# Performance work log

Hardware: AMD Instinct MI355X
Metric: run time of the kernel (lower is better)

## Reference

```python
import jax, jax.numpy as jnp
import numpy as np

K = 16                       # target expected number of distinct classes
NUM_LEVELS = 128             # num_discretization_levels
EPSILON = 0.1                # smoothing for derivative scales
NEWTON_ITERS = 3


def compute_normalizer(probs, k):
    """Solve for alpha s.t. sum_i (1 - exp(-alpha * p_i)) == k via Newton."""
    n = probs.shape[-1]
    alpha = jnp.full(probs.shape[:-1], float(k), dtype=probs.dtype)
    for _ in range(NEWTON_ITERS):
        e = jnp.exp(-alpha[..., None] * probs)          # (*, N)
        err = e.sum(axis=-1) + (k - n)                   # (*,)
        minus_d = (e * probs).sum(axis=-1)               # (*,)
        alpha = alpha + err / minus_d
    return alpha


def _derivative_scales(probs, eps):
    inv_p1 = 0.5 / (probs + eps)
    inv_p2 = 0.5 / (1.0 + eps - probs)
    common = eps * (inv_p1 + inv_p2)
    return inv_p1 + common, inv_p2 + common


@jax.custom_vjp
def fake_parameterized_dropout(probs, values, mask):
    return values * mask


def _fpd_fwd(probs, values, mask):
    return values * mask, (probs, values, mask)


def _fpd_bwd(res, g):
    probs, values, mask = res
    mask_grad = g * values
    s1, s2 = _derivative_scales(probs, EPSILON)
    probs_grad = mask_grad * (s1 * mask + s2 * (1.0 - mask))
    values_grad = g * mask
    return probs_grad, values_grad, jnp.zeros_like(mask)


fake_parameterized_dropout.defvjp(_fpd_fwd, _fpd_bwd)


def setup_inputs() -> dict:
    key = jax.random.key(0)
    k1, k2, k3, k4 = jax.random.split(key, 4)
    B, S, N = 4, 4096, 512
    return {
        "logits": jax.random.normal(k1, (B, S, N), dtype=jnp.float32),
        "values": jax.random.normal(k2, (B, S, N), dtype=jnp.float32),
        "u_mask": jax.random.uniform(k3, (B, S, N), dtype=jnp.float32),
        "u_disc": jax.random.uniform(k4, (B, S, N), dtype=jnp.float32),
    }


def reference(logits, values, u_mask, u_disc):
    probs = jax.nn.softmax(logits, axis=-1)                      # (*, N)
    alpha = compute_normalizer(probs, K)                         # (*,)
    # marginal prob of each class being chosen in K rounds
    marginals = 1.0 - (1.0 - probs) ** alpha[..., None]          # (*, N)
    # stochastic discretization with straight-through gradient
    idx = jnp.floor(marginals * (NUM_LEVELS - 1) + u_disc)
    y = idx * (1.0 / (NUM_LEVELS - 1))
    y_st = marginals + jax.lax.stop_gradient(y - marginals)
    # sample 0/1 mask with marginal probabilities y_st
    mask = (u_mask < y_st).astype(values.dtype)
    out = fake_parameterized_dropout(y_st, values, mask)
    return out
```

## Files before the change

kernel.cpp:

```cpp
#include <hip/hip_runtime.h>
#include <math.h>


#define ROW_N 512
#define EPW 16
constexpr double LEVELS_M1 = 127.0;
constexpr double INV_LEVELS_M1 = 1.0 / 127.0;

typedef float v4f __attribute__((ext_vector_type(4)));

template <int CTRL>
__device__ __forceinline__ float dpp_f32(float v) {
    int x = __builtin_amdgcn_update_dpp(0, __float_as_int(v), CTRL, 0xF, 0xF, true);
    return __int_as_float(x);
}
template <int CTRL>
__device__ __forceinline__ double dpp_f64(double v) {
    long long b = __double_as_longlong(v);
    int lo = __builtin_amdgcn_update_dpp(0, (int)(b & 0xFFFFFFFFLL), CTRL, 0xF, 0xF, true);
    int hi = __builtin_amdgcn_update_dpp(0, (int)(b >> 32),          CTRL, 0xF, 0xF, true);
    return __longlong_as_double(((long long)hi << 32) | (unsigned int)(unsigned)lo);
}

__device__ __forceinline__ double half_sum_f64(double v) {
    v += dpp_f64<0xB1>(v);
    v += dpp_f64<0x4E>(v);
    v += dpp_f64<0x141>(v);
    v += dpp_f64<0x140>(v);
    v += __shfl_xor(v, 16, 64);
    return v;
}
__device__ __forceinline__ float half_sum_f32(float v) {
    v += dpp_f32<0xB1>(v);
    v += dpp_f32<0x4E>(v);
    v += dpp_f32<0x141>(v);
    v += dpp_f32<0x140>(v);
    v += __shfl_xor(v, 16, 64);
    return v;
}

__device__ __forceinline__ double fast_recip1(double d) {
    double y = (double)__builtin_amdgcn_rcpf((float)d);
    return y * fma(-d, y, 2.0);
}

template <int DEG>
__device__ __forceinline__ double fast_exp(double x) {
    constexpr double C[12] = {
        1.0, 1.0, 0.5,
        1.6666666666666666574e-01,
        4.1666666666666664354e-02,
        8.3333333333333332177e-03,
        1.3888888888888889419e-03,
        1.9841269841269841253e-04,
        2.4801587301587301566e-05,
        2.7557319223985892511e-06,
        2.7557319223985888276e-07,
        2.5052108385441718775e-08
    };
    const double LOG2E = 1.4426950408889634074;
    const double LN2   = 6.9314718055994530942e-01;
    double kd = rint(x * LOG2E);
    double r  = fma(-kd, LN2, x);
    double p = C[DEG];
    #pragma unroll
    for (int k = DEG - 1; k >= 0; --k) p = fma(p, r, C[k]);
    long long sb = ((long long)(1023 + (int)kd)) << 52;
    return p * __longlong_as_double(sb);
}

__device__ __forceinline__ double fast_log1p(double r) {
    double u  = r * fast_recip1(2.0 + r);
    double u2 = u * u;
    double q = 2.0 / 9.0;
    q = fma(q, u2, 2.0 / 7.0);
    q = fma(q, u2, 2.0 / 5.0);
    q = fma(q, u2, 2.0 / 3.0);
    q = fma(q, u2, 2.0);
    return u * q;
}

__global__ __launch_bounds__(256)
void sbm_kernel(const float* __restrict__ logits,
                const float* __restrict__ values,
                const float* __restrict__ u_mask,
                const float* __restrict__ u_disc,
                float* __restrict__ out,
                int rows)
{
    const int wave = (int)((blockIdx.x * (unsigned)blockDim.x + threadIdx.x) >> 6);
    const int lane = (int)(threadIdx.x & 63u);
    if (2 * wave >= rows) return;

    const int half = lane >> 5;
    const int c    = lane & 31;

    const size_t pb = (size_t)wave * 256;
    const int    fi = half * 128 + c;

    const float4* l4 = (const float4*)logits + pb + fi;
    const float4* v4 = (const float4*)values + pb + fi;
    const float4* m4 = (const float4*)u_mask + pb + fi;
    const float4* d4 = (const float4*)u_disc + pb + fi;

    float4 lg[4], vv[4], um[4], ud[4];
    #pragma unroll
    for (int g = 0; g < 4; ++g) {
        lg[g] = l4[g * 32];
        vv[g] = v4[g * 32];
        um[g] = m4[g * 32];
        ud[g] = d4[g * 32];
    }

    double p[EPW];
    double s = 0.0;
    #pragma unroll
    for (int g = 0; g < 4; ++g) {
        const float lf[4] = {lg[g].x, lg[g].y, lg[g].z, lg[g].w};
        #pragma unroll
        for (int j = 0; j < 4; ++j) {
            p[g * 4 + j] = fast_exp<7>((double)lf[j]);
            s += p[g * 4 + j];
        }
    }
    s = half_sum_f64(s);
    const double inv_s = fast_recip1(s);
    float p32[EPW];
    #pragma unroll
    for (int i = 0; i < EPW; ++i) {
        p[i] *= inv_s;
        p32[i] = (float)p[i];
    }

    float se32 = 0.0f, sep32 = 0.0f;
    #pragma unroll
    for (int i = 0; i < EPW; ++i) {
        float e = __expf(-16.0f * p32[i]);
        se32 += e;
        sep32 = fmaf(e, p32[i], sep32);
    }
    se32  = half_sum_f32(se32);
    sep32 = half_sum_f32(sep32);
    const float a32 = 16.0f + (se32 - 496.0f) / sep32;

    double alpha = (double)a32;
    {
        double se = 0.0;
        float  sepf = 0.0f;
        #pragma unroll
        for (int i = 0; i < EPW; ++i) {
            double e = fast_exp<9>(-alpha * p[i]);
            se += e;
            sepf = fmaf((float)e, p32[i], sepf);
        }
        se   = half_sum_f64(se);
        sepf = half_sum_f32(sepf);
        alpha += (se - 496.0) * fast_recip1((double)sepf);
    }

    v4f* o4 = (v4f*)out + pb + fi;
    #pragma unroll
    for (int g = 0; g < 4; ++g) {
        const float vf[4] = {vv[g].x, vv[g].y, vv[g].z, vv[g].w};
        const float uf[4] = {um[g].x, um[g].y, um[g].z, um[g].w};
        const float df[4] = {ud[g].x, ud[g].y, ud[g].z, ud[g].w};
        v4f of;
        #pragma unroll
        for (int j = 0; j < 4; ++j) {
            const int i = g * 4 + j;
            const double t = 1.0 - p[i];
            const double r = t - 1.0;
            const double m = 1.0 - fast_exp<8>(alpha * fast_log1p(r));
            const double y = floor(fma(m, LEVELS_M1, (double)df[j])) * INV_LEVELS_M1;
            of[j] = ((double)uf[j] < y) ? vf[j] : 0.0f;
        }
        __builtin_nontemporal_store(of, o4 + g * 32);
    }
}

extern "C" void kernel_launch(void* const* d_in, const int* in_sizes, int n_in,
                              void* d_out, int out_size, void* d_ws, size_t ws_size,
                              hipStream_t stream) {
    const float* logits = (const float*)d_in[0];
    const float* values = (const float*)d_in[1];
    const float* u_mask = (const float*)d_in[2];
    const float* u_disc = (const float*)d_in[3];
    float* out = (float*)d_out;

    const int rows = in_sizes[0] / ROW_N;
    const int waves = rows / 2;
    const int block = 256;
    const int grid = (waves * 64 + block - 1) / block;

    sbm_kernel<<<grid, block, 0, stream>>>(logits, values, u_mask, u_disc, out, rows);
}
```

Measured before the change: 30.66 us.

## Process two row-pairs per wave with software-prefetched logits for next iteration

Each wave now handles two row-pairs, with the row-pairs spaced nwaves apart, and launches half as many waves. While the current row-pair is being computed, the logits for the next one are loaded ahead of time. The aim is to hide global load latency behind the heavy FP64 math and to cut launch and tail overhead. In exchange, register pressure rises and fewer waves are resident, so there is less latency hiding from occupancy. It also assumes rows divides evenly by 2*G_ITERS.

```diff
diff --git a/kernel.cpp b/kernel.cpp
--- a/kernel.cpp
+++ b/kernel.cpp
@@ -4,6 +4,7 @@
 
 #define ROW_N 512
 #define EPW 16
+#define G_ITERS 2
 constexpr double LEVELS_M1 = 127.0;
 constexpr double INV_LEVELS_M1 = 1.0 / 127.0;
 
@@ -86,95 +87,114 @@
                 const float* __restrict__ u_mask,
                 const float* __restrict__ u_disc,
                 float* __restrict__ out,
-                int rows)
+                int nwaves)
 {
     const int wave = (int)((blockIdx.x * (unsigned)blockDim.x + threadIdx.x) >> 6);
     const int lane = (int)(threadIdx.x & 63u);
-    if (2 * wave >= rows) return;
+    if (wave >= nwaves) return;
 
     const int half = lane >> 5;
     const int c    = lane & 31;
-
-    const size_t pb = (size_t)wave * 256;
-    const int    fi = half * 128 + c;
-
-    const float4* l4 = (const float4*)logits + pb + fi;
-    const float4* v4 = (const float4*)values + pb + fi;
-    const float4* m4 = (const float4*)u_mask + pb + fi;
-    const float4* d4 = (const float4*)u_disc + pb + fi;
-
-    float4 lg[4], vv[4], um[4], ud[4];
+    const int fi   = half * 128 + c;
+
+    size_t pb = (size_t)wave * 256;
+    float4 lgA[4];
+    {
+        const float4* l4 = (const float4*)logits + pb + fi;
+        #pragma unroll
+        for (int g = 0; g < 4; ++g) lgA[g] = l4[g * 32];
+    }
+
     #pragma unroll
-    for (int g = 0; g < 4; ++g) {
-        lg[g] = l4[g * 32];
-        vv[g] = v4[g * 32];
-        um[g] = m4[g * 32];
-        ud[g] = d4[g * 32];
-    }
-
-    double p[EPW];
-    double s = 0.0;
-    #pragma unroll
-    for (int g = 0; g < 4; ++g) {
-        const float lf[4] = {lg[g].x, lg[g].y, lg[g].z, lg[g].w};
-        #pragma unroll
-        for (int j = 0; j < 4; ++j) {
-            p[g * 4 + j] = fast_exp<7>((double)lf[j]);
-            s += p[g * 4 + j];
-        }
-    }
-    s = half_sum_f64(s);
-    const double inv_s = fast_recip1(s);
-    float p32[EPW];
-    #pragma unroll
-    for (int i = 0; i < EPW; ++i) {
-        p[i] *= inv_s;
-        p32[i] = (float)p[i];
-    }
-
-    float se32 = 0.0f, sep32 = 0.0f;
-    #pragma unroll
-    for (int i = 0; i < EPW; ++i) {
-        float e = __expf(-16.0f * p32[i]);
-        se32 += e;
-        sep32 = fmaf(e, p32[i], sep32);
-    }
-    se32  = half_sum_f32(se32);
-    sep32 = half_sum_f32(sep32);
-    const float a32 = 16.0f + (se32 - 496.0f) / sep32;
-
-    double alpha = (double)a32;
-    {
-        double se = 0.0;
-        float  sepf = 0.0f;
+    for (int it = 0; it < G_ITERS; ++it) {
+        float4 vv[4], um[4], ud[4];
+        {
+            const float4* v4 = (const float4*)values + pb + fi;
+            const float4* m4 = (const float4*)u_mask + pb + fi;
+            const float4* d4 = (const float4*)u_disc + pb + fi;
+            #pragma unroll
+            for (int g = 0; g < 4; ++g) {
+                vv[g] = v4[g * 32];
+                um[g] = m4[g * 32];
+                ud[g] = d4[g * 32];
+            }
+        }
+        const size_t pb_next = pb + (size_t)nwaves * 256;
+        float4 lgB[4];
+        if (it + 1 < G_ITERS) {
+            const float4* l4n = (const float4*)logits + pb_next + fi;
+            #pragma unroll
+            for (int g = 0; g < 4; ++g) lgB[g] = l4n[g * 32];
+        }
+
+        double p[EPW];
+        double s = 0.0;
+        #pragma unroll
+        for (int g = 0; g < 4; ++g) {
+            const float lf[4] = {lgA[g].x, lgA[g].y, lgA[g].z, lgA[g].w};
+            #pragma unroll
+            for (int j = 0; j < 4; ++j) {
+                p[g * 4 + j] = fast_exp<7>((double)lf[j]);
+                s += p[g * 4 + j];
+            }
+        }
+        s = half_sum_f64(s);
+        const double inv_s = fast_recip1(s);
+        float p32[EPW];
         #pragma unroll
         for (int i = 0; i < EPW; ++i) {
-            double e = fast_exp<9>(-alpha * p[i]);
-            se += e;
-            sepf = fmaf((float)e, p32[i], sepf);
-        }
-        se   = half_sum_f64(se);
-        sepf = half_sum_f32(sepf);
-        alpha += (se - 496.0) * fast_recip1((double)sepf);
-    }
-
-    v4f* o4 = (v4f*)out + pb + fi;
-    #pragma unroll
-    for (int g = 0; g < 4; ++g) {
-        const float vf[4] = {vv[g].x, vv[g].y, vv[g].z, vv[g].w};
-        const float uf[4] = {um[g].x, um[g].y, um[g].z, um[g].w};
-        const float df[4] = {ud[g].x, ud[g].y, ud[g].z, ud[g].w};
-        v4f of;
-        #pragma unroll
-        for (int j = 0; j < 4; ++j) {
-            const int i = g * 4 + j;
-            const double t = 1.0 - p[i];
-            const double r = t - 1.0;
-            const double m = 1.0 - fast_exp<8>(alpha * fast_log1p(r));
-            const double y = floor(fma(m, LEVELS_M1, (double)df[j])) * INV_LEVELS_M1;
-            of[j] = ((double)uf[j] < y) ? vf[j] : 0.0f;
-        }
-        __builtin_nontemporal_store(of, o4 + g * 32);
+            p[i] *= inv_s;
+            p32[i] = (float)p[i];
+        }
+
+        float se32 = 0.0f, sep32 = 0.0f;
+        #pragma unroll
+        for (int i = 0; i < EPW; ++i) {
+            float e = __expf(-16.0f * p32[i]);
+            se32 += e;
+            sep32 = fmaf(e, p32[i], sep32);
+        }
+        se32  = half_sum_f32(se32);
+        sep32 = half_sum_f32(sep32);
+        const float a32 = 16.0f + (se32 - 496.0f) / sep32;
+
+        double alpha = (double)a32;
+        {
+            double se = 0.0;
+            float  sepf = 0.0f;
+            #pragma unroll
+            for (int i = 0; i < EPW; ++i) {
+                double e = fast_exp<9>(-alpha * p[i]);
+                se += e;
+                sepf = fmaf((float)e, p32[i], sepf);
+            }
+            se   = half_sum_f64(se);
+            sepf = half_sum_f32(sepf);
+            alpha += (se - 496.0) * fast_recip1((double)sepf);
+        }
+
+        v4f* o4 = (v4f*)out + pb + fi;
+        #pragma unroll
+        for (int g = 0; g < 4; ++g) {
+            const float vf[4] = {vv[g].x, vv[g].y, vv[g].z, vv[g].w};
+            const float uf[4] = {um[g].x, um[g].y, um[g].z, um[g].w};
+            const float df[4] = {ud[g].x, ud[g].y, ud[g].z, ud[g].w};
+            v4f of;
+            #pragma unroll
+            for (int j = 0; j < 4; ++j) {
+                const int i = g * 4 + j;
+                const double t = 1.0 - p[i];
+                const double r = t - 1.0;
+                const double m = 1.0 - fast_exp<8>(alpha * fast_log1p(r));
+                const double y = floor(fma(m, LEVELS_M1, (double)df[j])) * INV_LEVELS_M1;
+                of[j] = ((double)uf[j] < y) ? vf[j] : 0.0f;
+            }
+            __builtin_nontemporal_store(of, o4 + g * 32);
+        }
+
+        pb = pb_next;
+        #pragma unroll
+        for (int g = 0; g < 4; ++g) lgA[g] = lgB[g];
     }
 }
 
@@ -188,9 +208,9 @@
     float* out = (float*)d_out;
 
     const int rows = in_sizes[0] / ROW_N;
-    const int waves = rows / 2;
+    const int nwaves = rows / 2 / G_ITERS;
     const int block = 256;
-    const int grid = (waves * 64 + block - 1) / block;
-
-    sbm_kernel<<<grid, block, 0, stream>>>(logits, values, u_mask, u_disc, out, rows);
-}
+    const int grid = (nwaves * 64 + block - 1) / block;
+
+    sbm_kernel<<<grid, block, 0, stream>>>(logits, values, u_mask, u_disc, out, nwaves);
+}
```

Result: slower. 31.34 us (+2.2%).

## Use cheap log1p polynomial for small probabilities and defer secondary loads

Applied to the files above, without the earlier changes.

Adds a wave-uniform branch: when every probability in the wave is below a threshold, log1p is evaluated with a short Taylor polynomial instead of the atanh form, which needs a reciprocal. The Newton-step exp polynomial degree is lowered from 9 to 7. The values/mask/disc loads are moved after the softmax exp computation, and the output store no longer uses the nontemporal hint. Together these aim to cut FP64 ALU work, at some accuracy risk near discretization boundaries and with some change in memory latency hiding.

```diff
diff --git a/kernel.cpp b/kernel.cpp
--- a/kernel.cpp
+++ b/kernel.cpp
@@ -69,7 +69,7 @@
     return p * __longlong_as_double(sb);
 }
 
-__device__ __forceinline__ double fast_log1p(double r) {
+__device__ __forceinline__ double log1p_atanh(double r) {
     double u  = r * fast_recip1(2.0 + r);
     double u2 = u * u;
     double q = 2.0 / 9.0;
@@ -78,6 +78,17 @@
     q = fma(q, u2, 2.0 / 3.0);
     q = fma(q, u2, 2.0);
     return u * q;
+}
+
+__device__ __forceinline__ double log1p_small(double r) {
+    double q = 1.0 / 7.0;
+    q = fma(q, r, -1.0 / 6.0);
+    q = fma(q, r,  1.0 / 5.0);
+    q = fma(q, r, -1.0 / 4.0);
+    q = fma(q, r,  1.0 / 3.0);
+    q = fma(q, r, -1.0 / 2.0);
+    q = fma(q, r,  1.0);
+    return r * q;
 }
 
 __global__ __launch_bounds__(256)
@@ -94,23 +105,13 @@
 
     const int half = lane >> 5;
     const int c    = lane & 31;
-
     const size_t pb = (size_t)wave * 256;
     const int    fi = half * 128 + c;
 
     const float4* l4 = (const float4*)logits + pb + fi;
-    const float4* v4 = (const float4*)values + pb + fi;
-    const float4* m4 = (const float4*)u_mask + pb + fi;
-    const float4* d4 = (const float4*)u_disc + pb + fi;
-
-    float4 lg[4], vv[4], um[4], ud[4];
-    #pragma unroll
-    for (int g = 0; g < 4; ++g) {
-        lg[g] = l4[g * 32];
-        vv[g] = v4[g * 32];
-        um[g] = m4[g * 32];
-        ud[g] = d4[g * 32];
-    }
+    float4 lg[4];
+    #pragma unroll
+    for (int g = 0; g < 4; ++g) lg[g] = l4[g * 32];
 
     double p[EPW];
     double s = 0.0;
@@ -123,13 +124,29 @@
             s += p[g * 4 + j];
         }
     }
+
+    float4 vv[4], um[4], ud[4];
+    {
+        const float4* v4 = (const float4*)values + pb + fi;
+        const float4* m4 = (const float4*)u_mask + pb + fi;
+        const float4* d4 = (const float4*)u_disc + pb + fi;
+        #pragma unroll
+        for (int g = 0; g < 4; ++g) {
+            vv[g] = v4[g * 32];
+            um[g] = m4[g * 32];
+            ud[g] = d4[g * 32];
+        }
+    }
+
     s = half_sum_f64(s);
     const double inv_s = fast_recip1(s);
     float p32[EPW];
+    float pmax = 0.0f;
     #pragma unroll
     for (int i = 0; i < EPW; ++i) {
         p[i] *= inv_s;
         p32[i] = (float)p[i];
+        pmax = fmaxf(pmax, p32[i]);
     }
 
     float se32 = 0.0f, sep32 = 0.0f;
@@ -149,13 +166,29 @@
         float  sepf = 0.0f;
         #pragma unroll
         for (int i = 0; i < EPW; ++i) {
-            double e = fast_exp<9>(-alpha * p[i]);
+            double e = fast_exp<7>(-alpha * p[i]);
             se += e;
             sepf = fmaf((float)e, p32[i], sepf);
         }
         se   = half_sum_f64(se);
         sepf = half_sum_f32(sepf);
         alpha += (se - 496.0) * fast_recip1((double)sepf);
+    }
+
+    const bool big = __any(pmax > 0.04f);
+    double L[EPW];
+    if (!big) {
+        #pragma unroll
+        for (int i = 0; i < EPW; ++i) {
+            const double t = 1.0 - p[i];
+            L[i] = log1p_small(t - 1.0);
+        }
+    } else {
+        #pragma unroll
+        for (int i = 0; i < EPW; ++i) {
+            const double t = 1.0 - p[i];
+            L[i] = log1p_atanh(t - 1.0);
+        }
     }
 
     v4f* o4 = (v4f*)out + pb + fi;
@@ -168,13 +201,11 @@
         #pragma unroll
         for (int j = 0; j < 4; ++j) {
             const int i = g * 4 + j;
-            const double t = 1.0 - p[i];
-            const double r = t - 1.0;
-            const double m = 1.0 - fast_exp<8>(alpha * fast_log1p(r));
+            const double m = 1.0 - fast_exp<8>(alpha * L[i]);
             const double y = floor(fma(m, LEVELS_M1, (double)df[j])) * INV_LEVELS_M1;
             of[j] = ((double)uf[j] < y) ? vf[j] : 0.0f;
         }
-        __builtin_nontemporal_store(of, o4 + g * 32);
+        *(o4 + g * 32) = of;
     }
 }
 
```

Measured after the change: 29.32 us. 4.4% less time.
